# Kernel optimization log

Measured on AMD Instinct MI355X. Metric: run time of the kernel, lower is better.

Reference implementation:

```python
import jax, jax.numpy as jnp
import numpy as np

N_U = 16          # |U| unary predicates
N_B = 8           # |B| binary predicates
N_NODES = 500000
N_EDGES = 2000000

# Parsed clause structure: (literal column indices, literal signs).
# Unary clauses over the |U|=16 unary predicate columns.
U_CLAUSES = [
    (np.array([0, 1]), np.array([-1.0, 1.0])),
    (np.array([2, 3]), np.array([-1.0, 1.0])),
    (np.array([4, 5, 6]), np.array([-1.0, 1.0, 1.0])),
]
# Binary clauses over the joined [2|U|+|B|]=40 space: x-copy offset 0, y-copy offset 16, binary offset 32.
B_CLAUSES = [
    (np.array([0, 16, 32]), np.array([-1.0, -1.0, 1.0])),
    (np.array([1, 17, 33]), np.array([-1.0, 1.0, 1.0])),
]


def knowledge_enhancer(x, clauses, weights):
    """KENN KnowledgeEnhancer with GodelBoostConormApprox boost.
    For each clause: delta = w * softmax(signed literals) * signs, scattered back.
    """
    delta = jnp.zeros_like(x)
    for (idx, sign), w in zip(clauses, weights):
        s = jnp.asarray(sign, x.dtype)
        v = x[:, idx] * s                      # [rows, clause_len]
        d = w * jax.nn.softmax(v, axis=-1) * s
        delta = delta.at[:, idx].add(d)
    return delta


def setup_inputs() -> dict:
    key = jax.random.key(0)
    k1, k2, k3, k4 = jax.random.split(key, 4)
    unary = jax.random.normal(k1, (N_NODES, N_U), jnp.float32)
    binary = jax.random.normal(k2, (N_EDGES, N_B), jnp.float32)
    edge_index = jax.random.randint(k3, (2, N_EDGES), 0, N_NODES)
    edge_weight = jax.random.uniform(k4, (N_EDGES,), jnp.float32)
    unary_clause_weights = jnp.full((len(U_CLAUSES),), 0.5, jnp.float32)
    binary_clause_weights = jnp.full((len(B_CLAUSES),), 0.5, jnp.float32)
    return {
        "unary": unary,
        "binary": binary,
        "edge_index": edge_index,
        "edge_weight": edge_weight,
        "unary_clause_weights": unary_clause_weights,
        "binary_clause_weights": binary_clause_weights,
    }


def reference(unary, binary, edge_index, edge_weight, unary_clause_weights, binary_clause_weights):
    i1, i2 = edge_index[0], edge_index[1]
    # unary KE
    u = unary + knowledge_enhancer(unary, U_CLAUSES, unary_clause_weights)
    # Join: gather both endpoints and concat with binary features -> [E, 2|U|+|B|]
    joined = jnp.concatenate([u[i1], u[i2], binary], axis=1)
    # binary KE, per-edge weighted
    d = knowledge_enhancer(joined, B_CLAUSES, binary_clause_weights) * edge_weight[:, None]
    ux = d[:, :N_U]
    uy = d[:, N_U:2 * N_U]
    db = d[:, 2 * N_U:]
    # GroupBy: indexed assignment (last-write semantics, matching torch tensor[index] = val)
    delta_up = jnp.zeros_like(u).at[i1].set(ux) + jnp.zeros_like(u).at[i2].set(uy)
    # activation is identity (default)
    return (u + delta_up, binary + db)
```

## Files before the change

### kernel.cpp

```cpp
#include <hip/hip_runtime.h>
#include <hip/hip_bf16.h>

typedef unsigned long long u64;

__device__ __forceinline__ float bf2f(unsigned short u) {
    union { unsigned int i; float f; } x; x.i = ((unsigned int)u) << 16; return x.f;
}
__device__ __forceinline__ unsigned short f2bf(float f) {
    union { float f; unsigned int i; } x; x.f = f;
    unsigned int r = x.i + 0x7fffu + ((x.i >> 16) & 1u);
    return (unsigned short)(r >> 16);
}

__device__ __forceinline__ bool detect_bf16(const void* unary) {
    const uint4* p = (const uint4*)unary;
    int plaus = 0;
    #pragma unroll
    for (int i = 0; i < 8; ++i) {
        uint4 v = p[i];
        unsigned int w[4] = {v.x, v.y, v.z, v.w};
        #pragma unroll
        for (int j = 0; j < 4; ++j) {
            int ex = (int)((w[j] >> 7) & 0xffu);
            if (ex >= 114 && ex <= 129) ++plaus;
        }
    }
    return plaus >= 16;
}

__device__ __forceinline__ float ldf(const void* p, size_t i, bool bf) {
    return bf ? bf2f(((const unsigned short*)p)[i]) : ((const float*)p)[i];
}


__global__ void f_init(const void* __restrict__ unary,
                       const void* __restrict__ wu,
                       unsigned int* __restrict__ u01,
                       u64* __restrict__ lastA,
                       u64* __restrict__ lastB,
                       int n_nodes)
{
    int n = blockIdx.x * blockDim.x + threadIdx.x;
    if (n >= n_nodes) return;
    bool bf = detect_bf16(unary);
    float x0 = ldf(unary, (size_t)n * 16 + 0, bf);
    float x1 = ldf(unary, (size_t)n * 16 + 1, bf);
    float w0 = ldf(wu, 0, bf);
    float t0 = __expf(-x0), t1 = __expf(x1), inv = w0 / (t0 + t1);
    x0 -= t0 * inv; x1 += t1 * inv;
    u01[n] = (unsigned int)f2bf(x0) | ((unsigned int)f2bf(x1) << 16);
    lastA[n] = 0ull;
    lastB[n] = 0ull;
}

__global__ void f_edge(const void* __restrict__ unary,
                       const void* __restrict__ binary,
                       const int*  __restrict__ ei,
                       const void* __restrict__ ew,
                       const void* __restrict__ wb,
                       const unsigned int* __restrict__ u01,
                       void* __restrict__ out0,
                       u64* __restrict__ lastA,
                       u64* __restrict__ lastB,
                       int n_nodes, int n_edges)
{
    int gid = blockIdx.x * blockDim.x + threadIdx.x;
    if (gid >= n_edges) return;
    int e = n_edges - 1 - gid;
    bool bf = detect_bf16(unary);
    size_t esz = bf ? 2u : 4u;
    char* out1 = (char*)out0 + (size_t)n_nodes * 16u * esz;

    int i1 = ei[e];
    int i2 = ei[e + n_edges];

    unsigned int pa = u01[i1];
    unsigned int pb = u01[i2];
    float a0 = bf2f((unsigned short)(pa & 0xffffu));
    float a1 = bf2f((unsigned short)(pa >> 16));
    float b0 = bf2f((unsigned short)(pb & 0xffffu));
    float b1 = bf2f((unsigned short)(pb >> 16));

    float c0 = ldf(binary, (size_t)e * 8 + 0, bf);
    float c1 = ldf(binary, (size_t)e * 8 + 1, bf);
    float w   = ldf(ew, e, bf);
    float wb0 = ldf(wb, 0, bf);
    float wb1 = ldf(wb, 1, bf);

    float tA0 = __expf(-a0), tA1 = __expf(-b0), tA2 = __expf(c0);
    float invA = w * wb0 / (tA0 + tA1 + tA2);
    float ux0 = -tA0 * invA, uy0 = -tA1 * invA, db0 = tA2 * invA;
    float tB0 = __expf(-a1), tB1 = __expf(b1), tB2 = __expf(c1);
    float invB = w * wb1 / (tB0 + tB1 + tB2);
    float ux1 = -tB0 * invB, uy1 = tB1 * invB, db1 = tB2 * invB;

    if (bf) {
        unsigned short el[8];
        *(uint4*)el = *(const uint4*)((const char*)binary + (size_t)e * 16);
        el[0] = f2bf(c0 + db0);
        el[1] = f2bf(c1 + db1);
        *(uint4*)(out1 + (size_t)e * 16) = *(uint4*)el;
    } else {
        const float* src = (const float*)binary + (size_t)e * 8;
        float r[8];
        *(uint4*)&r[0] = *(const uint4*)&src[0];
        *(uint4*)&r[4] = *(const uint4*)&src[4];
        r[0] = c0 + db0;
        r[1] = c1 + db1;
        float* dst = (float*)(out1 + (size_t)e * 32);
        *(uint4*)&dst[0] = *(uint4*)&r[0];
        *(uint4*)&dst[4] = *(uint4*)&r[4];
    }

    unsigned int key = (unsigned int)(e + 1);
    unsigned int qa = (unsigned int)f2bf(ux0) | ((unsigned int)f2bf(ux1) << 16);
    unsigned int qb = (unsigned int)f2bf(uy0) | ((unsigned int)f2bf(uy1) << 16);
    if ((unsigned int)(lastA[i1] >> 32) < key)
        atomicMax(&lastA[i1], ((u64)key << 32) | qa);
    if ((unsigned int)(lastB[i2] >> 32) < key)
        atomicMax(&lastB[i2], ((u64)key << 32) | qb);
}

__global__ void f_fin(const void* __restrict__ unary,
                      const void* __restrict__ wu,
                      const u64* __restrict__ lastA,
                      const u64* __restrict__ lastB,
                      void* __restrict__ out0,
                      int n_nodes)
{
    int n = blockIdx.x * blockDim.x + threadIdx.x;
    if (n >= n_nodes) return;
    bool bf = detect_bf16(unary);

    float x[16];
    if (bf) {
        const unsigned short* src = (const unsigned short*)unary + (size_t)n * 16;
        unsigned short el[16];
        *(uint4*)&el[0] = *(const uint4*)&src[0];
        *(uint4*)&el[8] = *(const uint4*)&src[8];
        #pragma unroll
        for (int i = 0; i < 16; ++i) x[i] = bf2f(el[i]);
    } else {
        const float* src = (const float*)unary + (size_t)n * 16;
        #pragma unroll
        for (int i = 0; i < 16; i += 4) *(uint4*)&x[i] = *(const uint4*)&src[i];
    }

    float w0 = ldf(wu, 0, bf), w1 = ldf(wu, 1, bf), w2 = ldf(wu, 2, bf);
    { float t0 = __expf(-x[0]), t1 = __expf(x[1]), inv = w0 / (t0 + t1);
      x[0] -= t0 * inv; x[1] += t1 * inv; }
    { float t0 = __expf(-x[2]), t1 = __expf(x[3]), inv = w1 / (t0 + t1);
      x[2] -= t0 * inv; x[3] += t1 * inv; }
    { float t0 = __expf(-x[4]), t1 = __expf(x[5]), t2 = __expf(x[6]);
      float inv = w2 / (t0 + t1 + t2);
      x[4] -= t0 * inv; x[5] += t1 * inv; x[6] += t2 * inv; }

    u64 sa = lastA[n], sb = lastB[n];
    if (sa) {
        x[0] += bf2f((unsigned short)(sa & 0xffffu));
        x[1] += bf2f((unsigned short)((sa >> 16) & 0xffffu));
    }
    if (sb) {
        x[0] += bf2f((unsigned short)(sb & 0xffffu));
        x[1] += bf2f((unsigned short)((sb >> 16) & 0xffffu));
    }

    if (bf) {
        unsigned short el[16];
        #pragma unroll
        for (int i = 0; i < 16; ++i) el[i] = f2bf(x[i]);
        uint4* dst = (uint4*)((char*)out0 + (size_t)n * 32);
        dst[0] = *(uint4*)&el[0];
        dst[1] = *(uint4*)&el[8];
    } else {
        float* dst = (float*)((char*)out0 + (size_t)n * 64);
        #pragma unroll
        for (int i = 0; i < 16; i += 4) *(uint4*)&dst[i] = *(uint4*)&x[i];
    }
}


__global__ void k_init(const void* __restrict__ unary, void* __restrict__ out0,
                       int n_nodes)
{
    int n = blockIdx.x * blockDim.x + threadIdx.x;
    if (n >= n_nodes) return;
    bool bf = detect_bf16(unary);
    size_t rs = bf ? 32u : 64u;
    u64* s = (u64*)((char*)out0 + (size_t)n * rs);
    s[0] = 0ull; s[1] = 0ull;
}

__global__ void k_edge(const void* __restrict__ unary,
                       const void* __restrict__ binary,
                       const int*  __restrict__ ei,
                       const void* __restrict__ ew,
                       const void* __restrict__ wu,
                       const void* __restrict__ wb,
                       void* __restrict__ out0,
                       int n_nodes, int n_edges)
{
    int e = blockIdx.x * blockDim.x + threadIdx.x;
    if (e >= n_edges) return;
    bool bf = detect_bf16(unary);
    size_t esz = bf ? 2u : 4u;
    size_t rs  = 16u * esz;
    char* out1 = (char*)out0 + (size_t)n_nodes * rs;

    int i1 = ei[e];
    int i2 = ei[e + n_edges];

    float w0 = ldf(wu, 0, bf);
    float a0 = ldf(unary, (size_t)i1 * 16 + 0, bf);
    float a1 = ldf(unary, (size_t)i1 * 16 + 1, bf);
    { float t0 = __expf(-a0), t1 = __expf(a1), inv = w0 / (t0 + t1);
      a0 -= t0 * inv; a1 += t1 * inv; }
    float b0 = ldf(unary, (size_t)i2 * 16 + 0, bf);
    float b1 = ldf(unary, (size_t)i2 * 16 + 1, bf);
    { float t0 = __expf(-b0), t1 = __expf(b1), inv = w0 / (t0 + t1);
      b0 -= t0 * inv; b1 += t1 * inv; }

    float c0 = ldf(binary, (size_t)e * 8 + 0, bf);
    float c1 = ldf(binary, (size_t)e * 8 + 1, bf);
    float w   = ldf(ew, e, bf);
    float wb0 = ldf(wb, 0, bf);
    float wb1 = ldf(wb, 1, bf);

    float tA0 = __expf(-a0), tA1 = __expf(-b0), tA2 = __expf(c0);
    float invA = w * wb0 / (tA0 + tA1 + tA2);
    float ux0 = -tA0 * invA, uy0 = -tA1 * invA, db0 = tA2 * invA;
    float tB0 = __expf(-a1), tB1 = __expf(b1), tB2 = __expf(c1);
    float invB = w * wb1 / (tB0 + tB1 + tB2);
    float ux1 = -tB0 * invB, uy1 = tB1 * invB, db1 = tB2 * invB;

    if (bf) {
        unsigned short el[8];
        *(uint4*)el = *(const uint4*)((const char*)binary + (size_t)e * 16);
        el[0] = f2bf(c0 + db0);
        el[1] = f2bf(c1 + db1);
        *(uint4*)(out1 + (size_t)e * 16) = *(uint4*)el;
    } else {
        const float* src = (const float*)binary + (size_t)e * 8;
        float r[8];
        *(uint4*)&r[0] = *(const uint4*)&src[0];
        *(uint4*)&r[4] = *(const uint4*)&src[4];
        r[0] = c0 + db0;
        r[1] = c1 + db1;
        float* dst = (float*)(out1 + (size_t)e * 32);
        *(uint4*)&dst[0] = *(uint4*)&r[0];
        *(uint4*)&dst[4] = *(uint4*)&r[4];
    }

    unsigned int pa = (unsigned int)f2bf(ux0) | ((unsigned int)f2bf(ux1) << 16);
    unsigned int pb = (unsigned int)f2bf(uy0) | ((unsigned int)f2bf(uy1) << 16);
    u64 ka = ((u64)(unsigned int)(e + 1) << 32) | pa;
    u64 kb = ((u64)(unsigned int)(e + 1) << 32) | pb;
    atomicMax((u64*)((char*)out0 + (size_t)i1 * rs),     ka);
    atomicMax((u64*)((char*)out0 + (size_t)i2 * rs + 8), kb);
}

__global__ void k_fin(const void* __restrict__ unary,
                      const void* __restrict__ wu,
                      void* __restrict__ out0,
                      int n_nodes)
{
    int n = blockIdx.x * blockDim.x + threadIdx.x;
    if (n >= n_nodes) return;
    bool bf = detect_bf16(unary);
    size_t rs = bf ? 32u : 64u;
    char* row = (char*)out0 + (size_t)n * rs;

    u64 sa = ((const u64*)row)[0];
    u64 sb = ((const u64*)row)[1];

    float x[16];
    if (bf) {
        const unsigned short* src = (const unsigned short*)unary + (size_t)n * 16;
        unsigned short el[16];
        *(uint4*)&el[0] = *(const uint4*)&src[0];
        *(uint4*)&el[8] = *(const uint4*)&src[8];
        #pragma unroll
        for (int i = 0; i < 16; ++i) x[i] = bf2f(el[i]);
    } else {
        const float* src = (const float*)unary + (size_t)n * 16;
        #pragma unroll
        for (int i = 0; i < 16; i += 4) *(uint4*)&x[i] = *(const uint4*)&src[i];
    }

    float w0 = ldf(wu, 0, bf), w1 = ldf(wu, 1, bf), w2 = ldf(wu, 2, bf);
    { float t0 = __expf(-x[0]), t1 = __expf(x[1]), inv = w0 / (t0 + t1);
      x[0] -= t0 * inv; x[1] += t1 * inv; }
    { float t0 = __expf(-x[2]), t1 = __expf(x[3]), inv = w1 / (t0 + t1);
      x[2] -= t0 * inv; x[3] += t1 * inv; }
    { float t0 = __expf(-x[4]), t1 = __expf(x[5]), t2 = __expf(x[6]);
      float inv = w2 / (t0 + t1 + t2);
      x[4] -= t0 * inv; x[5] += t1 * inv; x[6] += t2 * inv; }

    if (sa) {
        x[0] += bf2f((unsigned short)(sa & 0xffffu));
        x[1] += bf2f((unsigned short)((sa >> 16) & 0xffffu));
    }
    if (sb) {
        x[0] += bf2f((unsigned short)(sb & 0xffffu));
        x[1] += bf2f((unsigned short)((sb >> 16) & 0xffffu));
    }

    if (bf) {
        unsigned short el[16];
        #pragma unroll
        for (int i = 0; i < 16; ++i) el[i] = f2bf(x[i]);
        uint4* dst = (uint4*)row;
        dst[0] = *(uint4*)&el[0];
        dst[1] = *(uint4*)&el[8];
    } else {
        float* dst = (float*)row;
        #pragma unroll
        for (int i = 0; i < 16; i += 4) *(uint4*)&dst[i] = *(uint4*)&x[i];
    }
}

extern "C" void kernel_launch(void* const* d_in, const int* in_sizes, int n_in,
                              void* d_out, int out_size, void* d_ws, size_t ws_size,
                              hipStream_t stream)
{
    const void* unary  = d_in[0];
    const void* binary = d_in[1];
    const int*  ei     = (const int*)d_in[2];
    const void* ew     = d_in[3];
    const void* wu     = d_in[4];
    const void* wb     = d_in[5];

    const int n_nodes = in_sizes[0] / 16;
    const int n_edges = in_sizes[1] / 8;

    const int B = 256;
    const size_t need = (size_t)n_nodes * (4 + 8 + 8);

    if (ws_size >= need) {
        unsigned int* u01 = (unsigned int*)d_ws;
        u64* lastA = (u64*)((char*)d_ws + (size_t)n_nodes * 4);
        u64* lastB = lastA + n_nodes;
        f_init<<<(n_nodes + B - 1) / B, B, 0, stream>>>(
            unary, wu, u01, lastA, lastB, n_nodes);
        f_edge<<<(n_edges + B - 1) / B, B, 0, stream>>>(
            unary, binary, ei, ew, wb, u01, d_out, lastA, lastB,
            n_nodes, n_edges);
        f_fin<<<(n_nodes + B - 1) / B, B, 0, stream>>>(
            unary, wu, lastA, lastB, d_out, n_nodes);
    } else {
        k_init<<<(n_nodes + B - 1) / B, B, 0, stream>>>(unary, d_out, n_nodes);
        k_edge<<<(n_edges + B - 1) / B, B, 0, stream>>>(
            unary, binary, ei, ew, wu, wb, d_out, n_nodes, n_edges);
        k_fin<<<(n_nodes + B - 1) / B, B, 0, stream>>>(unary, wu, d_out, n_nodes);
    }
}
```

Baseline: 159.3 us.

## Replace global last-write atomics with node-binned record scatter and per-bin LDS reduction

```diff
diff --git a/kernel.cpp b/kernel.cpp
--- a/kernel.cpp
+++ b/kernel.cpp
@@ -2,13 +2,14 @@
 #include <hip/hip_bf16.h>
 
 typedef unsigned long long u64;
+typedef unsigned int u32;
 
 __device__ __forceinline__ float bf2f(unsigned short u) {
-    union { unsigned int i; float f; } x; x.i = ((unsigned int)u) << 16; return x.f;
+    union { u32 i; float f; } x; x.i = ((u32)u) << 16; return x.f;
 }
 __device__ __forceinline__ unsigned short f2bf(float f) {
-    union { float f; unsigned int i; } x; x.f = f;
-    unsigned int r = x.i + 0x7fffu + ((x.i >> 16) & 1u);
+    union { float f; u32 i; } x; x.f = f;
+    u32 r = x.i + 0x7fffu + ((x.i >> 16) & 1u);
     return (unsigned short)(r >> 16);
 }
 
@@ -18,7 +19,7 @@
     #pragma unroll
     for (int i = 0; i < 8; ++i) {
         uint4 v = p[i];
-        unsigned int w[4] = {v.x, v.y, v.z, v.w};
+        u32 w[4] = {v.x, v.y, v.z, v.w};
         #pragma unroll
         for (int j = 0; j < 4; ++j) {
             int ex = (int)((w[j] >> 7) & 0xffu);
@@ -32,99 +33,229 @@
     return bf ? bf2f(((const unsigned short*)p)[i]) : ((const float*)p)[i];
 }
 
-
-__global__ void f_init(const void* __restrict__ unary,
-                       const void* __restrict__ wu,
-                       unsigned int* __restrict__ u01,
-                       u64* __restrict__ lastA,
-                       u64* __restrict__ lastB,
-                       int n_nodes)
-{
-    int n = blockIdx.x * blockDim.x + threadIdx.x;
-    if (n >= n_nodes) return;
-    bool bf = detect_bf16(unary);
-    float x0 = ldf(unary, (size_t)n * 16 + 0, bf);
-    float x1 = ldf(unary, (size_t)n * 16 + 1, bf);
-    float w0 = ldf(wu, 0, bf);
-    float t0 = __expf(-x0), t1 = __expf(x1), inv = w0 / (t0 + t1);
-    x0 -= t0 * inv; x1 += t1 * inv;
-    u01[n] = (unsigned int)f2bf(x0) | ((unsigned int)f2bf(x1) << 16);
-    lastA[n] = 0ull;
-    lastB[n] = 0ull;
-}
-
-__global__ void f_edge(const void* __restrict__ unary,
-                       const void* __restrict__ binary,
-                       const int*  __restrict__ ei,
-                       const void* __restrict__ ew,
-                       const void* __restrict__ wb,
-                       const unsigned int* __restrict__ u01,
-                       void* __restrict__ out0,
-                       u64* __restrict__ lastA,
-                       u64* __restrict__ lastB,
-                       int n_nodes, int n_edges)
-{
-    int gid = blockIdx.x * blockDim.x + threadIdx.x;
-    if (gid >= n_edges) return;
-    int e = n_edges - 1 - gid;
-    bool bf = detect_bf16(unary);
-    size_t esz = bf ? 2u : 4u;
-    char* out1 = (char*)out0 + (size_t)n_nodes * 16u * esz;
-
-    int i1 = ei[e];
-    int i2 = ei[e + n_edges];
-
-    unsigned int pa = u01[i1];
-    unsigned int pb = u01[i2];
+__device__ __forceinline__ void edge_math(u32 pa, u32 pb, float c0, float c1,
+                                          float w, float wb0, float wb1,
+                                          u32& qa, u32& qb,
+                                          float& o0, float& o1)
+{
     float a0 = bf2f((unsigned short)(pa & 0xffffu));
     float a1 = bf2f((unsigned short)(pa >> 16));
     float b0 = bf2f((unsigned short)(pb & 0xffffu));
     float b1 = bf2f((unsigned short)(pb >> 16));
-
-    float c0 = ldf(binary, (size_t)e * 8 + 0, bf);
-    float c1 = ldf(binary, (size_t)e * 8 + 1, bf);
-    float w   = ldf(ew, e, bf);
-    float wb0 = ldf(wb, 0, bf);
-    float wb1 = ldf(wb, 1, bf);
-
     float tA0 = __expf(-a0), tA1 = __expf(-b0), tA2 = __expf(c0);
     float invA = w * wb0 / (tA0 + tA1 + tA2);
     float ux0 = -tA0 * invA, uy0 = -tA1 * invA, db0 = tA2 * invA;
     float tB0 = __expf(-a1), tB1 = __expf(b1), tB2 = __expf(c1);
     float invB = w * wb1 / (tB0 + tB1 + tB2);
     float ux1 = -tB0 * invB, uy1 = tB1 * invB, db1 = tB2 * invB;
-
-    if (bf) {
-        unsigned short el[8];
-        *(uint4*)el = *(const uint4*)((const char*)binary + (size_t)e * 16);
-        el[0] = f2bf(c0 + db0);
-        el[1] = f2bf(c1 + db1);
-        *(uint4*)(out1 + (size_t)e * 16) = *(uint4*)el;
-    } else {
-        const float* src = (const float*)binary + (size_t)e * 8;
-        float r[8];
-        *(uint4*)&r[0] = *(const uint4*)&src[0];
-        *(uint4*)&r[4] = *(const uint4*)&src[4];
-        r[0] = c0 + db0;
-        r[1] = c1 + db1;
-        float* dst = (float*)(out1 + (size_t)e * 32);
-        *(uint4*)&dst[0] = *(uint4*)&r[0];
-        *(uint4*)&dst[4] = *(uint4*)&r[4];
-    }
-
-    unsigned int key = (unsigned int)(e + 1);
-    unsigned int qa = (unsigned int)f2bf(ux0) | ((unsigned int)f2bf(ux1) << 16);
-    unsigned int qb = (unsigned int)f2bf(uy0) | ((unsigned int)f2bf(uy1) << 16);
-    if ((unsigned int)(lastA[i1] >> 32) < key)
-        atomicMax(&lastA[i1], ((u64)key << 32) | qa);
-    if ((unsigned int)(lastB[i2] >> 32) < key)
-        atomicMax(&lastB[i2], ((u64)key << 32) | qb);
-}
-
-__global__ void f_fin(const void* __restrict__ unary,
+    qa = (u32)f2bf(ux0) | ((u32)f2bf(ux1) << 16);
+    qb = (u32)f2bf(uy0) | ((u32)f2bf(uy1) << 16);
+    o0 = c0 + db0; o1 = c1 + db1;
+}
+
+#define BIN_SHIFT 11
+#define MAXBINS 256
+#define EPB 4096
+
+__global__ void r_init(const void* __restrict__ unary,
+                       const void* __restrict__ wu,
+                       u32* __restrict__ u01,
+                       u64* __restrict__ winA,
+                       u64* __restrict__ winB,
+                       u32* __restrict__ histA,
+                       u32* __restrict__ histB,
+                       int n_nodes)
+{
+    int n = blockIdx.x * blockDim.x + threadIdx.x;
+    if (n >= n_nodes) return;
+    if (n < MAXBINS) { histA[n] = 0u; histB[n] = 0u; }
+    bool bf = detect_bf16(unary);
+    float x0 = ldf(unary, (size_t)n * 16 + 0, bf);
+    float x1 = ldf(unary, (size_t)n * 16 + 1, bf);
+    float w0 = ldf(wu, 0, bf);
+    float t0 = __expf(-x0), t1 = __expf(x1), inv = w0 / (t0 + t1);
+    x0 -= t0 * inv; x1 += t1 * inv;
+    u01[n] = (u32)f2bf(x0) | ((u32)f2bf(x1) << 16);
+    winA[n] = 0ull;
+    winB[n] = 0ull;
+}
+
+__global__ __launch_bounds__(256) void r_count(const int* __restrict__ ei,
+                                               u32* __restrict__ histA,
+                                               u32* __restrict__ histB,
+                                               int n_edges, int nbins)
+{
+    __shared__ u32 hA[MAXBINS], hB[MAXBINS];
+    int tid = threadIdx.x;
+    for (int b = tid; b < MAXBINS; b += 256) { hA[b] = 0u; hB[b] = 0u; }
+    __syncthreads();
+    size_t e0 = (size_t)blockIdx.x * EPB;
+    #pragma unroll
+    for (int k = 0; k < EPB / 256; ++k) {
+        size_t e = e0 + (size_t)k * 256 + tid;
+        if (e < (size_t)n_edges) {
+            atomicAdd(&hA[(u32)ei[e] >> BIN_SHIFT], 1u);
+            atomicAdd(&hB[(u32)ei[e + n_edges] >> BIN_SHIFT], 1u);
+        }
+    }
+    __syncthreads();
+    for (int b = tid; b < nbins; b += 256) {
+        if (hA[b]) atomicAdd(&histA[b], hA[b]);
+        if (hB[b]) atomicAdd(&histB[b], hB[b]);
+    }
+}
+
+__global__ __launch_bounds__(256) void r_scan(const u32* __restrict__ histA,
+                                              const u32* __restrict__ histB,
+                                              u32* __restrict__ baseA,
+                                              u32* __restrict__ baseB,
+                                              u32* __restrict__ curA,
+                                              u32* __restrict__ curB,
+                                              int nbins)
+{
+    __shared__ u32 s[MAXBINS];
+    int tid = threadIdx.x;
+    u32 vA = (tid < nbins) ? histA[tid] : 0u;
+    s[tid] = vA; __syncthreads();
+    for (int off = 1; off < 256; off <<= 1) {
+        u32 v = (tid >= off) ? s[tid - off] : 0u;
+        __syncthreads(); s[tid] += v; __syncthreads();
+    }
+    if (tid < nbins) { u32 ex = s[tid] - vA; baseA[tid] = ex; curA[tid] = ex; }
+    __syncthreads();
+    u32 vB = (tid < nbins) ? histB[tid] : 0u;
+    s[tid] = vB; __syncthreads();
+    for (int off = 1; off < 256; off <<= 1) {
+        u32 v = (tid >= off) ? s[tid - off] : 0u;
+        __syncthreads(); s[tid] += v; __syncthreads();
+    }
+    if (tid < nbins) { u32 ex = s[tid] - vB; baseB[tid] = ex; curB[tid] = ex; }
+}
+
+__global__ __launch_bounds__(256) void r_scatter(
+        const void* __restrict__ unary,
+        const void* __restrict__ binary,
+        const int*  __restrict__ ei,
+        const void* __restrict__ ew,
+        const void* __restrict__ wb,
+        const u32* __restrict__ u01,
+        void* __restrict__ out0,
+        u32* __restrict__ curA,
+        u32* __restrict__ curB,
+        u64* __restrict__ recA,
+        u64* __restrict__ recB,
+        int n_nodes, int n_edges, int nbins)
+{
+    __shared__ u32 cA[MAXBINS], cB[MAXBINS], bA[MAXBINS], bB[MAXBINS];
+    int tid = threadIdx.x;
+    for (int b = tid; b < MAXBINS; b += 256) { cA[b] = 0u; cB[b] = 0u; }
+    __syncthreads();
+    size_t e0 = (size_t)blockIdx.x * EPB;
+
+    #pragma unroll
+    for (int k = 0; k < EPB / 256; ++k) {
+        size_t e = e0 + (size_t)k * 256 + tid;
+        if (e < (size_t)n_edges) {
+            atomicAdd(&cA[(u32)ei[e] >> BIN_SHIFT], 1u);
+            atomicAdd(&cB[(u32)ei[e + n_edges] >> BIN_SHIFT], 1u);
+        }
+    }
+    __syncthreads();
+    for (int b = tid; b < nbins; b += 256) {
+        u32 c = cA[b]; if (c) bA[b] = atomicAdd(&curA[b], c);
+        u32 d = cB[b]; if (d) bB[b] = atomicAdd(&curB[b], d);
+    }
+    __syncthreads();
+    for (int b = tid; b < MAXBINS; b += 256) { cA[b] = 0u; cB[b] = 0u; }
+    __syncthreads();
+
+    bool bf = detect_bf16(unary);
+    float wb0 = ldf(wb, 0, bf);
+    float wb1 = ldf(wb, 1, bf);
+    char* out1 = (char*)out0 + (size_t)n_nodes * 16u * (bf ? 2u : 4u);
+
+    #pragma unroll
+    for (int k = 0; k < EPB / 256; ++k) {
+        size_t e = e0 + (size_t)k * 256 + tid;
+        if (e >= (size_t)n_edges) continue;
+        u32 i1 = (u32)ei[e];
+        u32 i2 = (u32)ei[e + n_edges];
+        u32 pa = u01[i1];
+        u32 pb = u01[i2];
+        float w = ldf(ew, e, bf);
+        u32 qa, qb; float o0, o1;
+
+        if (bf) {
+            uint4 row = *(const uint4*)((const char*)binary + e * 16);
+            float c0 = bf2f((unsigned short)(row.x & 0xffffu));
+            float c1 = bf2f((unsigned short)(row.x >> 16));
+            edge_math(pa, pb, c0, c1, w, wb0, wb1, qa, qb, o0, o1);
+            row.x = (u32)f2bf(o0) | ((u32)f2bf(o1) << 16);
+            *(uint4*)(out1 + e * 16) = row;
+        } else {
+            const float* src = (const float*)binary + e * 8;
+            uint4 r0 = *(const uint4*)&src[0];
+            uint4 r1 = *(const uint4*)&src[4];
+            float c0 = __uint_as_float(r0.x);
+            float c1 = __uint_as_float(r0.y);
+            edge_math(pa, pb, c0, c1, w, wb0, wb1, qa, qb, o0, o1);
+            r0.x = __float_as_uint(o0);
+            r0.y = __float_as_uint(o1);
+            float* dst = (float*)(out1 + e * 32);
+            *(uint4*)&dst[0] = r0;
+            *(uint4*)&dst[4] = r1;
+        }
+
+        u64 key = (u64)(e + 1);
+        u32 binA = i1 >> BIN_SHIFT, binB = i2 >> BIN_SHIFT;
+        u32 rA = atomicAdd(&cA[binA], 1u);
+        u32 rB = atomicAdd(&cB[binB], 1u);
+        recA[bA[binA] + rA] = (key << 43) | ((u64)(i1 & 2047u) << 32) | qa;
+        recB[bB[binB] + rB] = (key << 43) | ((u64)(i2 & 2047u) << 32) | qb;
+    }
+}
+
+__global__ __launch_bounds__(256) void r_reduce(
+        const u64* __restrict__ recA,
+        const u64* __restrict__ recB,
+        const u32* __restrict__ baseA,
+        const u32* __restrict__ baseB,
+        const u32* __restrict__ histA,
+        const u32* __restrict__ histB,
+        u64* __restrict__ winA,
+        u64* __restrict__ winB,
+        int nbins)
+{
+    __shared__ u32 kmax[1 << BIN_SHIFT];
+    int tid = threadIdx.x;
+    int blk = blockIdx.x;
+    bool sideB = (blk >= nbins);
+    int bin = sideB ? blk - nbins : blk;
+    const u64* rec = sideB ? recB : recA;
+    u32 lo  = sideB ? baseB[bin] : baseA[bin];
+    u32 cnt = sideB ? histB[bin] : histA[bin];
+    u64* win = sideB ? winB : winA;
+
+    for (int i = tid; i < (1 << BIN_SHIFT); i += 256) kmax[i] = 0u;
+    __syncthreads();
+    for (u32 r = tid; r < cnt; r += 256) {
+        u64 rc = rec[lo + r];
+        atomicMax(&kmax[(u32)(rc >> 32) & 2047u], (u32)(rc >> 43));
+    }
+    __syncthreads();
+    for (u32 r = tid; r < cnt; r += 256) {
+        u64 rc = rec[lo + r];
+        u32 nl  = (u32)(rc >> 32) & 2047u;
+        u32 key = (u32)(rc >> 43);
+        if (key == kmax[nl])
+            win[((size_t)bin << BIN_SHIFT) + nl] = ((u64)key << 32) | (u32)rc;
+    }
+}
+
+__global__ void r_fin(const void* __restrict__ unary,
                       const void* __restrict__ wu,
-                      const u64* __restrict__ lastA,
-                      const u64* __restrict__ lastB,
+                      const u64* __restrict__ winA,
+                      const u64* __restrict__ winB,
                       void* __restrict__ out0,
                       int n_nodes)
 {
@@ -155,7 +286,7 @@
       float inv = w2 / (t0 + t1 + t2);
       x[4] -= t0 * inv; x[5] += t1 * inv; x[6] += t2 * inv; }
 
-    u64 sa = lastA[n], sb = lastB[n];
+    u64 sa = winA[n], sb = winB[n];
     if (sa) {
         x[0] += bf2f((unsigned short)(sa & 0xffffu));
         x[1] += bf2f((unsigned short)((sa >> 16) & 0xffffu));
@@ -176,6 +307,91 @@
         float* dst = (float*)((char*)out0 + (size_t)n * 64);
         #pragma unroll
         for (int i = 0; i < 16; i += 4) *(uint4*)&dst[i] = *(uint4*)&x[i];
+    }
+}
+
+
+__global__ void f_init(const void* __restrict__ unary,
+                       const void* __restrict__ wu,
+                       u32* __restrict__ u01,
+                       u64* __restrict__ lastA,
+                       u64* __restrict__ lastB,
+                       u32* __restrict__ shA,
+                       u32* __restrict__ shB,
+                       int n_nodes)
+{
+    int n = blockIdx.x * blockDim.x + threadIdx.x;
+    if (n >= n_nodes) return;
+    bool bf = detect_bf16(unary);
+    float x0 = ldf(unary, (size_t)n * 16 + 0, bf);
+    float x1 = ldf(unary, (size_t)n * 16 + 1, bf);
+    float w0 = ldf(wu, 0, bf);
+    float t0 = __expf(-x0), t1 = __expf(x1), inv = w0 / (t0 + t1);
+    x0 -= t0 * inv; x1 += t1 * inv;
+    u01[n] = (u32)f2bf(x0) | ((u32)f2bf(x1) << 16);
+    lastA[n] = 0ull;
+    lastB[n] = 0ull;
+    shA[n] = 0u;
+    shB[n] = 0u;
+}
+
+__global__ void f_edge(const void* __restrict__ unary,
+                       const void* __restrict__ binary,
+                       const int*  __restrict__ ei,
+                       const void* __restrict__ ew,
+                       const void* __restrict__ wb,
+                       const u32* __restrict__ u01,
+                       void* __restrict__ out0,
+                       u64* __restrict__ lastA,
+                       u64* __restrict__ lastB,
+                       u32* __restrict__ shA,
+                       u32* __restrict__ shB,
+                       int n_nodes, int n_edges)
+{
+    int gid = blockIdx.x * blockDim.x + threadIdx.x;
+    if (gid >= n_edges) return;
+    int e = n_edges - 1 - gid;
+    bool bf = detect_bf16(unary);
+    char* out1 = (char*)out0 + (size_t)n_nodes * 16u * (bf ? 2u : 4u);
+
+    u32 i1 = (u32)ei[e];
+    u32 i2 = (u32)ei[e + n_edges];
+    u32 pa = u01[i1];
+    u32 pb = u01[i2];
+    float w   = ldf(ew, e, bf);
+    float wb0 = ldf(wb, 0, bf);
+    float wb1 = ldf(wb, 1, bf);
+    u32 qa, qb; float o0, o1;
+
+    if (bf) {
+        uint4 row = *(const uint4*)((const char*)binary + (size_t)e * 16);
+        float c0 = bf2f((unsigned short)(row.x & 0xffffu));
+        float c1 = bf2f((unsigned short)(row.x >> 16));
+        edge_math(pa, pb, c0, c1, w, wb0, wb1, qa, qb, o0, o1);
+        row.x = (u32)f2bf(o0) | ((u32)f2bf(o1) << 16);
+        *(uint4*)(out1 + (size_t)e * 16) = row;
+    } else {
+        const float* src = (const float*)binary + (size_t)e * 8;
+        uint4 r0 = *(const uint4*)&src[0];
+        uint4 r1 = *(const uint4*)&src[4];
+        float c0 = __uint_as_float(r0.x);
+        float c1 = __uint_as_float(r0.y);
+        edge_math(pa, pb, c0, c1, w, wb0, wb1, qa, qb, o0, o1);
+        r0.x = __float_as_uint(o0);
+        r0.y = __float_as_uint(o1);
+        float* dst = (float*)(out1 + (size_t)e * 32);
+        *(uint4*)&dst[0] = r0;
+        *(uint4*)&dst[4] = r1;
+    }
+
+    u32 key = (u32)(e + 1);
+    if (shA[i1] < key) {
+        shA[i1] = key;
+        atomicMax(&lastA[i1], ((u64)key << 32) | qa);
+    }
+    if (shB[i2] < key) {
+        shB[i2] = key;
+        atomicMax(&lastB[i2], ((u64)key << 32) | qb);
     }
 }
 
@@ -203,13 +419,11 @@
     int e = blockIdx.x * blockDim.x + threadIdx.x;
     if (e >= n_edges) return;
     bool bf = detect_bf16(unary);
-    size_t esz = bf ? 2u : 4u;
-    size_t rs  = 16u * esz;
+    size_t rs = 16u * (bf ? 2u : 4u);
     char* out1 = (char*)out0 + (size_t)n_nodes * rs;
 
-    int i1 = ei[e];
-    int i2 = ei[e + n_edges];
-
+    u32 i1 = (u32)ei[e];
+    u32 i2 = (u32)ei[e + n_edges];
     float w0 = ldf(wu, 0, bf);
     float a0 = ldf(unary, (size_t)i1 * 16 + 0, bf);
     float a1 = ldf(unary, (size_t)i1 * 16 + 1, bf);
@@ -219,42 +433,37 @@
     float b1 = ldf(unary, (size_t)i2 * 16 + 1, bf);
     { float t0 = __expf(-b0), t1 = __expf(b1), inv = w0 / (t0 + t1);
       b0 -= t0 * inv; b1 += t1 * inv; }
-
-    float c0 = ldf(binary, (size_t)e * 8 + 0, bf);
-    float c1 = ldf(binary, (size_t)e * 8 + 1, bf);
+    u32 pa = (u32)f2bf(a0) | ((u32)f2bf(a1) << 16);
+    u32 pb = (u32)f2bf(b0) | ((u32)f2bf(b1) << 16);
+
     float w   = ldf(ew, e, bf);
     float wb0 = ldf(wb, 0, bf);
     float wb1 = ldf(wb, 1, bf);
-
-    float tA0 = __expf(-a0), tA1 = __expf(-b0), tA2 = __expf(c0);
-    float invA = w * wb0 / (tA0 + tA1 + tA2);
-    float ux0 = -tA0 * invA, uy0 = -tA1 * invA, db0 = tA2 * invA;
-    float tB0 = __expf(-a1), tB1 = __expf(b1), tB2 = __expf(c1);
-    float invB = w * wb1 / (tB0 + tB1 + tB2);
-    float ux1 = -tB0 * invB, uy1 = tB1 * invB, db1 = tB2 * invB;
+    u32 qa, qb; float o0, o1;
 
     if (bf) {
-        unsigned short el[8];
-        *(uint4*)el = *(const uint4*)((const char*)binary + (size_t)e * 16);
-        el[0] = f2bf(c0 + db0);
-        el[1] = f2bf(c1 + db1);
-        *(uint4*)(out1 + (size_t)e * 16) = *(uint4*)el;
+        uint4 row = *(const uint4*)((const char*)binary + (size_t)e * 16);
+        float c0 = bf2f((unsigned short)(row.x & 0xffffu));
+        float c1 = bf2f((unsigned short)(row.x >> 16));
+        edge_math(pa, pb, c0, c1, w, wb0, wb1, qa, qb, o0, o1);
+        row.x = (u32)f2bf(o0) | ((u32)f2bf(o1) << 16);
+        *(uint4*)(out1 + (size_t)e * 16) = row;
     } else {
         const float* src = (const float*)binary + (size_t)e * 8;
-        float r[8];
-        *(uint4*)&r[0] = *(const uint4*)&src[0];
-        *(uint4*)&r[4] = *(const uint4*)&src[4];
-        r[0] = c0 + db0;
-        r[1] = c1 + db1;
+        uint4 r0 = *(const uint4*)&src[0];
+        uint4 r1 = *(const uint4*)&src[4];
+        float c0 = __uint_as_float(r0.x);
+        float c1 = __uint_as_float(r0.y);
+        edge_math(pa, pb, c0, c1, w, wb0, wb1, qa, qb, o0, o1);
+        r0.x = __float_as_uint(o0);
+        r0.y = __float_as_uint(o1);
         float* dst = (float*)(out1 + (size_t)e * 32);
-        *(uint4*)&dst[0] = *(uint4*)&r[0];
-        *(uint4*)&dst[4] = *(uint4*)&r[4];
-    }
-
-    unsigned int pa = (unsigned int)f2bf(ux0) | ((unsigned int)f2bf(ux1) << 16);
-    unsigned int pb = (unsigned int)f2bf(uy0) | ((unsigned int)f2bf(uy1) << 16);
-    u64 ka = ((u64)(unsigned int)(e + 1) << 32) | pa;
-    u64 kb = ((u64)(unsigned int)(e + 1) << 32) | pb;
+        *(uint4*)&dst[0] = r0;
+        *(uint4*)&dst[4] = r1;
+    }
+
+    u64 ka = ((u64)(u32)(e + 1) << 32) | qa;
+    u64 kb = ((u64)(u32)(e + 1) << 32) | qb;
     atomicMax((u64*)((char*)out0 + (size_t)i1 * rs),     ka);
     atomicMax((u64*)((char*)out0 + (size_t)i2 * rs + 8), kb);
 }
@@ -269,7 +478,6 @@
     bool bf = detect_bf16(unary);
     size_t rs = bf ? 32u : 64u;
     char* row = (char*)out0 + (size_t)n * rs;
-
     u64 sa = ((const u64*)row)[0];
     u64 sb = ((const u64*)row)[1];
 
@@ -332,20 +540,54 @@
 
     const int n_nodes = in_sizes[0] / 16;
     const int n_edges = in_sizes[1] / 8;
-
     const int B = 256;
-    const size_t need = (size_t)n_nodes * (4 + 8 + 8);
-
-    if (ws_size >= need) {
-        unsigned int* u01 = (unsigned int*)d_ws;
+
+    const int nbins = (n_nodes + (1 << BIN_SHIFT) - 1) >> BIN_SHIFT;
+
+    const size_t off_win  = (size_t)n_nodes * 4;
+    const size_t off_hist = off_win + (size_t)n_nodes * 16;
+    const size_t off_rec  = off_hist + (size_t)MAXBINS * 6 * 4;
+    const size_t need_r   = off_rec + (size_t)n_edges * 16;
+    const size_t need_f   = (size_t)n_nodes * (4 + 8 + 8 + 4 + 4);
+
+    if (ws_size >= need_r && nbins <= MAXBINS &&
+        (n_nodes % 2 == 0) && n_edges < (1 << 21)) {
+        u32* u01  = (u32*)d_ws;
+        u64* winA = (u64*)((char*)d_ws + off_win);
+        u64* winB = winA + n_nodes;
+        u32* histA = (u32*)((char*)d_ws + off_hist);
+        u32* histB = histA + MAXBINS;
+        u32* baseA = histB + MAXBINS;
+        u32* baseB = baseA + MAXBINS;
+        u32* curA  = baseB + MAXBINS;
+        u32* curB  = curA + MAXBINS;
+        u64* recA = (u64*)((char*)d_ws + off_rec);
+        u64* recB = recA + n_edges;
+
+        int nb_e = (n_edges + EPB - 1) / EPB;
+        r_init<<<(n_nodes + B - 1) / B, B, 0, stream>>>(
+            unary, wu, u01, winA, winB, histA, histB, n_nodes);
+        r_count<<<nb_e, B, 0, stream>>>(ei, histA, histB, n_edges, nbins);
+        r_scan<<<1, B, 0, stream>>>(histA, histB, baseA, baseB, curA, curB, nbins);
+        r_scatter<<<nb_e, B, 0, stream>>>(
+            unary, binary, ei, ew, wb, u01, d_out, curA, curB, recA, recB,
+            n_nodes, n_edges, nbins);
+        r_reduce<<<2 * nbins, B, 0, stream>>>(
+            recA, recB, baseA, baseB, histA, histB, winA, winB, nbins);
+        r_fin<<<(n_nodes + B - 1) / B, B, 0, stream>>>(
+            unary, wu, winA, winB, d_out, n_nodes);
+    } else if (ws_size >= need_f) {
+        u32* u01 = (u32*)d_ws;
         u64* lastA = (u64*)((char*)d_ws + (size_t)n_nodes * 4);
         u64* lastB = lastA + n_nodes;
+        u32* shA = (u32*)(lastB + n_nodes);
+        u32* shB = shA + n_nodes;
         f_init<<<(n_nodes + B - 1) / B, B, 0, stream>>>(
-            unary, wu, u01, lastA, lastB, n_nodes);
+            unary, wu, u01, lastA, lastB, shA, shB, n_nodes);
         f_edge<<<(n_edges + B - 1) / B, B, 0, stream>>>(
-            unary, binary, ei, ew, wb, u01, d_out, lastA, lastB,
+            unary, binary, ei, ew, wb, u01, d_out, lastA, lastB, shA, shB,
             n_nodes, n_edges);
-        f_fin<<<(n_nodes + B - 1) / B, B, 0, stream>>>(
+        r_fin<<<(n_nodes + B - 1) / B, B, 0, stream>>>(
             unary, wu, lastA, lastB, d_out, n_nodes);
     } else {
         k_init<<<(n_nodes + B - 1) / B, B, 0, stream>>>(unary, d_out, n_nodes);
```

Result: no change. 162.4 us (+2.0%).
